# Kernel tuning notes

Measured on AMD Instinct MI355X. Metric: run time of the kernel, lower is better.

## Reference

```python
import jax, jax.numpy as jnp
import numpy as np

P = 16          # patch_size
EMBED = 768     # embed_dim
HEAD_DIM = 64   # embed_dim // num_heads
ROPE_BASE = 10000.0


def rope_2d(coords, head_dim, base):
    """Axial 2D RoPE. coords: (N, 2) int -> cos, sin each (N, head_dim).
    head_dim is split evenly over the two axes; within an axis, frequency
    pairs are repeated twice (standard rotate-pairs layout)."""
    dpa = head_dim // 2                                   # dims per axis
    inv_freq = 1.0 / (base ** (jnp.arange(0, dpa, 2, dtype=jnp.float32) / dpa))  # (dpa//2,)
    ang = coords.astype(jnp.float32)[:, :, None] * inv_freq[None, None, :]       # (N, 2, dpa//2)
    ang = jnp.repeat(ang, 2, axis=-1).reshape(coords.shape[0], head_dim)          # (N, head_dim)
    return jnp.cos(ang), jnp.sin(ang)


def setup_inputs() -> dict:
    key = jax.random.key(0)
    k1, k2 = jax.random.split(key, 2)
    B, C, H, W = 32, 3, 512, 512
    images = jax.random.normal(k1, (B, C, H, W), dtype=jnp.float32)
    patch_dim = C * P * P
    W_proj = jax.random.normal(k2, (patch_dim, EMBED), dtype=jnp.float32) * (patch_dim ** -0.5)
    b_proj = jnp.zeros((EMBED,), dtype=jnp.float32)
    return {"images": images, "W_proj": W_proj, "b_proj": b_proj}


def reference(images, W_proj, b_proj):
    B, C, H, W = images.shape
    Hp, Wp = H // P, W // P
    N = B * Hp * Wp
    # patchify: c (hp p1) (wp p2) -> (hp wp) (c p1 p2), packed across batch
    x = images.reshape(B, C, Hp, P, Wp, P).transpose(0, 2, 4, 1, 3, 5).reshape(N, C * P * P)
    tokens = x @ W_proj + b_proj                              # (N, EMBED)
    # per-image patch coordinates (identical grid for every image)
    ys, xs = jnp.meshgrid(jnp.arange(Hp), jnp.arange(Wp), indexing='ij')
    coords = jnp.stack([ys, xs], axis=-1).reshape(Hp * Wp, 2)
    patch_coords = jnp.tile(coords, (B, 1))                    # (N, 2)
    rope_cos, rope_sin = rope_2d(patch_coords, HEAD_DIM, ROPE_BASE)
    cu_seqlens = (jnp.arange(B + 1, dtype=jnp.int32) * (Hp * Wp))
    is_patch = jnp.ones((N,), dtype=bool)
    return tokens, cu_seqlens, patch_coords, rope_cos, rope_sin, is_patch
```

## Files before the change

kernel.cpp:

```cpp
#include <hip/hip_runtime.h>
#include <hip/hip_bf16.h>

typedef unsigned short u16;
typedef unsigned int   u32;
typedef __bf16 bf16x8 __attribute__((ext_vector_type(8)));
typedef float  f32x4  __attribute__((ext_vector_type(4)));

#define N_TOK 32768
constexpr long long OFF_TOKENS = 0;
constexpr long long OFF_CU     = 25165824LL;
constexpr long long OFF_COORDS = 25165857LL;
constexpr long long OFF_COS    = 25231393LL;
constexpr long long OFF_SIN    = 27328545LL;
constexpr long long OFF_ISP    = 29425697LL;

__device__ __forceinline__ void split_bf16(float v, u16& h, u16& l) {
    __hip_bfloat16 bh = __float2bfloat16(v);
    float fh = __bfloat162float(bh);
    __hip_bfloat16 bl = __float2bfloat16(v - fh);
    h = __builtin_bit_cast(u16, bh);
    l = __builtin_bit_cast(u16, bl);
}

__device__ __forceinline__ u32 pk2(float lo, float hi) {
    u32 a = (u32)__builtin_bit_cast(u16, __float2bfloat16(lo));
    u32 b = (u32)__builtin_bit_cast(u16, __float2bfloat16(hi));
    return a | (b << 16);
}

__global__ __launch_bounds__(256) void prep_w(const float* __restrict__ W,
                                              u16* __restrict__ wt2) {
    const int bid = blockIdx.x;
    const int bn  = bid / 24;
    const int kt  = bid - bn * 24;
    __shared__ u16 im[8192];
    const int t  = threadIdx.x;
    const int k  = t >> 3;
    const int n0 = (t & 7) * 16;
    const float* src = W + (size_t)(kt * 32 + k) * 768 + bn * 128 + n0;
    #pragma unroll
    for (int e = 0; e < 16; e++) {
        const int n = n0 + e;
        u16 h, l;
        split_bf16(src[e], h, l);
        const int p = (n * 64 + (((k >> 4) ^ ((n >> 3) & 1)) << 5) + (k & 15) * 2) >> 1;
        im[p] = h;
        im[4096 + p] = l;
    }
    __syncthreads();
    uint4* g = (uint4*)(wt2 + (size_t)bid * 8192);
    const uint4* s = (const uint4*)im;
    #pragma unroll
    for (int i = 0; i < 4; i++) g[t + i * 256] = s[t + i * 256];
}

__global__ __launch_bounds__(512, 4) void patch_gemm_mfma(
    const float* __restrict__ img, const u16* __restrict__ wt2,
    const float* __restrict__ bias, float* __restrict__ out)
{
    __shared__ __align__(16) char smem[49152];
    char* pA0 = smem;
    char* pA1 = smem + 8192;
    char* pB0 = smem + 16384;
    char* pB1 = smem + 32768;

    const int L   = blockIdx.x;
    const int c   = (L & 7) * 192 + (L >> 3);
    const int bm  = c / 6;
    const int bn  = c - bm * 6;
    const int tb  = bn * 24;

    const int tid  = threadIdx.x;
    const int lane = tid & 63;
    const int wid  = tid >> 6;
    const int wm   = (wid >> 2) << 6;
    const int wn   = (wid & 3) << 5;
    const int lr   = lane & 15;
    const int lg   = lane >> 4;

    const int am = tid & 127;
    const int aq = tid >> 7;
    const int m  = bm * 128 + am;
    const int bb = m >> 10;
    const int hp = (m & 1023) >> 5;
    const int wq = m & 31;
    const float* abase = img + (size_t)bb * 786432 + (size_t)hp * 8192 + wq * 16;
    const int a_wb = am * 64 + (((aq >> 1) ^ ((am >> 3) & 1)) << 5) + ((aq & 1) << 4);

    const int a_rd = lr * 64 + (((lg >> 1) ^ ((lr >> 3) & 1)) << 5) + ((lg & 1) << 4);

    f32x4 acc[4][2];
    #pragma unroll
    for (int i = 0; i < 4; i++)
        #pragma unroll
        for (int j = 0; j < 2; j++) acc[i][j] = {0.f, 0.f, 0.f, 0.f};

    float4 A0a, A0b, A1a, A1b;

#define LOAD_A(ra, rb, T)                                                   \
    {   const float* ap = abase + ((T) >> 3) * 262144 +                     \
            (((T) & 7) * 2 + (aq >> 1)) * 512 + (aq & 1) * 8;               \
        ra = *(const float4*)ap;  rb = *(const float4*)(ap + 4); }

#define CVT_STORE(ra, rb, pdst)                                             \
    {   uint4 Hq;                                                           \
        Hq.x = pk2(ra.x, ra.y); Hq.y = pk2(ra.z, ra.w);                     \
        Hq.z = pk2(rb.x, rb.y); Hq.w = pk2(rb.z, rb.w);                     \
        *(uint4*)((pdst) + a_wb) = Hq; }

#define GLOADB(T, dst)                                                      \
    {   const char* s = (const char*)wt2 + (size_t)(tb + (T)) * 16384       \
                        + (wid << 11) + (lane << 4);                        \
        char* d = (dst) + (wid << 11);                                      \
        __builtin_amdgcn_global_load_lds(                                   \
            (const __attribute__((address_space(1))) u32*)s,                \
            (__attribute__((address_space(3))) u32*)d, 16, 0, 0);           \
        __builtin_amdgcn_global_load_lds(                                   \
            (const __attribute__((address_space(1))) u32*)(s + 1024),       \
            (__attribute__((address_space(3))) u32*)(d + 1024), 16, 0, 0); }

#define COMPUTE(pAc, pBc)                                                   \
    {   bf16x8 ahf[4], bhf[2], blf[2];                                      \
        _Pragma("unroll")                                                   \
        for (int i = 0; i < 4; i++)                                         \
            ahf[i] = *(const bf16x8*)((pAc) + ((wm + i * 16) << 6) + a_rd); \
        _Pragma("unroll")                                                   \
        for (int j = 0; j < 2; j++) {                                       \
            bhf[j] = *(const bf16x8*)((pBc) + ((wn + j * 16) << 6) + a_rd); \
            blf[j] = *(const bf16x8*)((pBc) + 8192 + ((wn + j * 16) << 6) + a_rd); \
        }                                                                   \
        _Pragma("unroll")                                                   \
        for (int i = 0; i < 4; i++)                                         \
            _Pragma("unroll")                                               \
            for (int j = 0; j < 2; j++) {                                   \
                acc[i][j] = __builtin_amdgcn_mfma_f32_16x16x32_bf16(ahf[i], bhf[j], acc[i][j], 0, 0, 0); \
                acc[i][j] = __builtin_amdgcn_mfma_f32_16x16x32_bf16(ahf[i], blf[j], acc[i][j], 0, 0, 0); \
            } }

    LOAD_A(A0a, A0b, 0);
    GLOADB(0, pB0);
    LOAD_A(A1a, A1b, 1);
    CVT_STORE(A0a, A0b, pA0);
    __syncthreads();

    #pragma unroll 1
    for (int t = 0; t < 24; t += 2) {
        if (t < 23) { CVT_STORE(A1a, A1b, pA1); GLOADB(t + 1, pB1); }
        if (t < 22) LOAD_A(A0a, A0b, t + 2);
        COMPUTE(pA0, pB0);
        __syncthreads();
        if (t + 1 < 23) { CVT_STORE(A0a, A0b, pA0); GLOADB(t + 2, pB0); }
        if (t + 1 < 22) LOAD_A(A1a, A1b, t + 3);
        COMPUTE(pA1, pB1);
        __syncthreads();
    }
#undef LOAD_A
#undef CVT_STORE
#undef GLOADB
#undef COMPUTE

    float bv[2];
    #pragma unroll
    for (int j = 0; j < 2; j++) bv[j] = bias[bn * 128 + wn + j * 16 + lr];
    #pragma unroll
    for (int i = 0; i < 4; i++) {
        const int rb = bm * 128 + wm + i * 16 + lg * 4;
        #pragma unroll
        for (int j = 0; j < 2; j++) {
            const int cg = bn * 128 + wn + j * 16 + lr;
            #pragma unroll
            for (int r = 0; r < 4; r++)
                out[OFF_TOKENS + (size_t)(rb + r) * 768 + cg] = acc[i][j][r] + bv[j];
        }
    }
}

__global__ __launch_bounds__(256) void aux_kernel(float* __restrict__ out)
{
    const int idx = blockIdx.x * 256 + threadIdx.x;
    if (idx >= N_TOK * 32) return;
    const int n  = idx >> 5;
    const int jd = idx & 31;

    const int hp = (n & 1023) >> 5;
    const int wp = n & 31;

    const int coord = (jd < 16) ? hp : wp;
    const int j = jd & 15;
    const float freq = exp2f(-(float)j * 0.8304820237218406f);
    float s, c;
    sincosf((float)coord * freq, &s, &c);

    const long long off = (long long)n * 64 + jd * 2;
    *(float2*)(out + OFF_COS + off) = make_float2(c, c);
    *(float2*)(out + OFF_SIN + off) = make_float2(s, s);

    if (jd == 0) {
        out[OFF_COORDS + 2 * (long long)n]     = (float)hp;
        out[OFF_COORDS + 2 * (long long)n + 1] = (float)wp;
        out[OFF_ISP + n] = 1.0f;
    }
    if (jd == 1 && n < 33) {
        out[OFF_CU + n] = (float)(n * 1024);
    }
}

extern "C" void kernel_launch(void* const* d_in, const int* in_sizes, int n_in,
                              void* d_out, int out_size, void* d_ws, size_t ws_size,
                              hipStream_t stream) {
    const float* img  = (const float*)d_in[0];
    const float* W    = (const float*)d_in[1];
    const float* bias = (const float*)d_in[2];
    float* out = (float*)d_out;
    u16* wt2 = (u16*)d_ws;

    prep_w<<<144, 256, 0, stream>>>(W, wt2);

    patch_gemm_mfma<<<1536, 512, 0, stream>>>(img, wt2, bias, out);

    const int aux_elems = N_TOK * 32;
    aux_kernel<<<(aux_elems + 255) / 256, 256, 0, stream>>>(out);
}
```

Before: 266.8 us.

## Triple-buffer GEMM LDS tiles with deeper prefetch and explicit waitcnt barriers

```diff
diff --git a/kernel.cpp b/kernel.cpp
--- a/kernel.cpp
+++ b/kernel.cpp
@@ -58,11 +58,13 @@
     const float* __restrict__ img, const u16* __restrict__ wt2,
     const float* __restrict__ bias, float* __restrict__ out)
 {
-    __shared__ __align__(16) char smem[49152];
+    __shared__ __align__(16) char smem[73728];
     char* pA0 = smem;
     char* pA1 = smem + 8192;
-    char* pB0 = smem + 16384;
-    char* pB1 = smem + 32768;
+    char* pA2 = smem + 16384;
+    char* pB0 = smem + 24576;
+    char* pB1 = smem + 40960;
+    char* pB2 = smem + 57344;
 
     const int L   = blockIdx.x;
     const int c   = (L & 7) * 192 + (L >> 3);
@@ -95,7 +97,7 @@
         #pragma unroll
         for (int j = 0; j < 2; j++) acc[i][j] = {0.f, 0.f, 0.f, 0.f};
 
-    float4 A0a, A0b, A1a, A1b;
+    float4 A0a, A0b, A1a, A1b, A2a, A2b;
 
 #define LOAD_A(ra, rb, T)                                                   \
     {   const float* ap = abase + ((T) >> 3) * 262144 +                     \
@@ -137,23 +139,32 @@
                 acc[i][j] = __builtin_amdgcn_mfma_f32_16x16x32_bf16(ahf[i], blf[j], acc[i][j], 0, 0, 0); \
             } }
 
+#define ITER(T, Ca, Cb, La, Lb, PACV, PBGL, PAC, PBC)                       \
+    {   if ((T) + 1 < 24) CVT_STORE(Ca, Cb, PACV);                          \
+        if ((T) + 2 < 24) GLOADB((T) + 2, PBGL);                            \
+        __builtin_amdgcn_sched_barrier(0);                                  \
+        if ((T) + 3 < 24) LOAD_A(La, Lb, (T) + 3);                          \
+        COMPUTE(PAC, PBC);                                                  \
+        asm volatile("s_waitcnt vmcnt(6) lgkmcnt(0)" ::: "memory");         \
+        __builtin_amdgcn_s_barrier();                                       \
+    }
+
+    GLOADB(0, pB0);
     LOAD_A(A0a, A0b, 0);
-    GLOADB(0, pB0);
+    GLOADB(1, pB1);
     LOAD_A(A1a, A1b, 1);
+    LOAD_A(A2a, A2b, 2);
     CVT_STORE(A0a, A0b, pA0);
-    __syncthreads();
+    asm volatile("s_waitcnt vmcnt(6) lgkmcnt(0)" ::: "memory");
+    __builtin_amdgcn_s_barrier();
 
     #pragma unroll 1
-    for (int t = 0; t < 24; t += 2) {
-        if (t < 23) { CVT_STORE(A1a, A1b, pA1); GLOADB(t + 1, pB1); }
-        if (t < 22) LOAD_A(A0a, A0b, t + 2);
-        COMPUTE(pA0, pB0);
-        __syncthreads();
-        if (t + 1 < 23) { CVT_STORE(A0a, A0b, pA0); GLOADB(t + 2, pB0); }
-        if (t + 1 < 22) LOAD_A(A1a, A1b, t + 3);
-        COMPUTE(pA1, pB1);
-        __syncthreads();
-    }
+    for (int t = 0; t < 24; t += 3) {
+        ITER(t,     A1a, A1b, A0a, A0b, pA1, pB2, pA0, pB0);
+        ITER(t + 1, A2a, A2b, A1a, A1b, pA2, pB0, pA1, pB1);
+        ITER(t + 2, A0a, A0b, A2a, A2b, pA0, pB1, pA2, pB2);
+    }
+#undef ITER
 #undef LOAD_A
 #undef CVT_STORE
 #undef GLOADB
```

After: 263.1 us. About the same (-1.4%).

## Load W fragments directly from global into registers, dropping B LDS staging

Applied to the files above, without the earlier changes.

```diff
diff --git a/kernel.cpp b/kernel.cpp
--- a/kernel.cpp
+++ b/kernel.cpp
@@ -33,36 +33,37 @@
     const int bid = blockIdx.x;
     const int bn  = bid / 24;
     const int kt  = bid - bn * 24;
-    __shared__ u16 im[8192];
-    const int t  = threadIdx.x;
-    const int k  = t >> 3;
-    const int n0 = (t & 7) * 16;
-    const float* src = W + (size_t)(kt * 32 + k) * 768 + bn * 128 + n0;
-    #pragma unroll
-    for (int e = 0; e < 16; e++) {
-        const int n = n0 + e;
-        u16 h, l;
-        split_bf16(src[e], h, l);
-        const int p = (n * 64 + (((k >> 4) ^ ((n >> 3) & 1)) << 5) + (k & 15) * 2) >> 1;
-        im[p] = h;
-        im[4096 + p] = l;
-    }
-    __syncthreads();
-    uint4* g = (uint4*)(wt2 + (size_t)bid * 8192);
-    const uint4* s = (const uint4*)im;
-    #pragma unroll
-    for (int i = 0; i < 4; i++) g[t + i * 256] = s[t + i * 256];
+    const int t   = threadIdx.x;
+    #pragma unroll
+    for (int p = 0; p < 2; p++) {
+        const int idx  = t + p * 256;
+        const int lane = idx & 63;
+        const int j    = (idx >> 6) & 1;
+        const int wnq  = idx >> 7;
+        const int n    = bn * 128 + wnq * 32 + j * 16 + (lane & 15);
+        const int k0   = kt * 32 + (lane >> 4) * 8;
+        u16 hv[8], lv[8];
+        #pragma unroll
+        for (int e = 0; e < 8; e++)
+            split_bf16(W[(size_t)(k0 + e) * 768 + n], hv[e], lv[e]);
+        uint4 H, L;
+        H.x = (u32)hv[0] | ((u32)hv[1] << 16); H.y = (u32)hv[2] | ((u32)hv[3] << 16);
+        H.z = (u32)hv[4] | ((u32)hv[5] << 16); H.w = (u32)hv[6] | ((u32)hv[7] << 16);
+        L.x = (u32)lv[0] | ((u32)lv[1] << 16); L.y = (u32)lv[2] | ((u32)lv[3] << 16);
+        L.z = (u32)lv[4] | ((u32)lv[5] << 16); L.w = (u32)lv[6] | ((u32)lv[7] << 16);
+        u16* dst = wt2 + (size_t)bid * 8192 + (((wnq << 12) | (j << 10) | (lane << 4)) >> 1);
+        *(uint4*)dst          = H;
+        *(uint4*)(dst + 1024) = L;
+    }
 }
 
 __global__ __launch_bounds__(512, 4) void patch_gemm_mfma(
     const float* __restrict__ img, const u16* __restrict__ wt2,
     const float* __restrict__ bias, float* __restrict__ out)
 {
-    __shared__ __align__(16) char smem[49152];
+    __shared__ __align__(16) char smem[16384];
     char* pA0 = smem;
     char* pA1 = smem + 8192;
-    char* pB0 = smem + 16384;
-    char* pB1 = smem + 32768;
 
     const int L   = blockIdx.x;
     const int c   = (L & 7) * 192 + (L >> 3);
@@ -89,6 +90,8 @@
 
     const int a_rd = lr * 64 + (((lg >> 1) ^ ((lr >> 3) & 1)) << 5) + ((lg & 1) << 4);
 
+    const char* bfrag = (const char*)wt2 + ((wid & 3) << 12) + (lane << 4);
+
     f32x4 acc[4][2];
     #pragma unroll
     for (int i = 0; i < 4; i++)
@@ -108,56 +111,44 @@
         Hq.z = pk2(rb.x, rb.y); Hq.w = pk2(rb.z, rb.w);                     \
         *(uint4*)((pdst) + a_wb) = Hq; }
 
-#define GLOADB(T, dst)                                                      \
-    {   const char* s = (const char*)wt2 + (size_t)(tb + (T)) * 16384       \
-                        + (wid << 11) + (lane << 4);                        \
-        char* d = (dst) + (wid << 11);                                      \
-        __builtin_amdgcn_global_load_lds(                                   \
-            (const __attribute__((address_space(1))) u32*)s,                \
-            (__attribute__((address_space(3))) u32*)d, 16, 0, 0);           \
-        __builtin_amdgcn_global_load_lds(                                   \
-            (const __attribute__((address_space(1))) u32*)(s + 1024),       \
-            (__attribute__((address_space(3))) u32*)(d + 1024), 16, 0, 0); }
-
-#define COMPUTE(pAc, pBc)                                                   \
-    {   bf16x8 ahf[4], bhf[2], blf[2];                                      \
+#define ITER(T, Ca, Cb, La, Lb, PACV, PAC)                                  \
+    {   bf16x8 bhf[2], blf[2];                                              \
+        {   const char* s = bfrag + (size_t)(tb + (T)) * 16384;             \
+            bhf[0] = *(const bf16x8*)(s);                                   \
+            bhf[1] = *(const bf16x8*)(s + 1024);                            \
+            blf[0] = *(const bf16x8*)(s + 2048);                            \
+            blf[1] = *(const bf16x8*)(s + 3072); }                          \
+        if ((T) + 1 < 24) CVT_STORE(Ca, Cb, PACV);                          \
+        if ((T) + 2 < 24) LOAD_A(La, Lb, (T) + 2);                          \
+        bf16x8 ahf[4];                                                      \
         _Pragma("unroll")                                                   \
         for (int i = 0; i < 4; i++)                                         \
-            ahf[i] = *(const bf16x8*)((pAc) + ((wm + i * 16) << 6) + a_rd); \
-        _Pragma("unroll")                                                   \
-        for (int j = 0; j < 2; j++) {                                       \
-            bhf[j] = *(const bf16x8*)((pBc) + ((wn + j * 16) << 6) + a_rd); \
-            blf[j] = *(const bf16x8*)((pBc) + 8192 + ((wn + j * 16) << 6) + a_rd); \
-        }                                                                   \
+            ahf[i] = *(const bf16x8*)((PAC) + ((wm + i * 16) << 6) + a_rd); \
         _Pragma("unroll")                                                   \
         for (int i = 0; i < 4; i++)                                         \
             _Pragma("unroll")                                               \
             for (int j = 0; j < 2; j++) {                                   \
                 acc[i][j] = __builtin_amdgcn_mfma_f32_16x16x32_bf16(ahf[i], bhf[j], acc[i][j], 0, 0, 0); \
                 acc[i][j] = __builtin_amdgcn_mfma_f32_16x16x32_bf16(ahf[i], blf[j], acc[i][j], 0, 0, 0); \
-            } }
+            }                                                               \
+        asm volatile("s_waitcnt lgkmcnt(0)" ::: "memory");                  \
+        __builtin_amdgcn_s_barrier();                                       \
+    }
 
     LOAD_A(A0a, A0b, 0);
-    GLOADB(0, pB0);
     LOAD_A(A1a, A1b, 1);
     CVT_STORE(A0a, A0b, pA0);
-    __syncthreads();
+    asm volatile("s_waitcnt lgkmcnt(0)" ::: "memory");
+    __builtin_amdgcn_s_barrier();
 
     #pragma unroll 1
     for (int t = 0; t < 24; t += 2) {
-        if (t < 23) { CVT_STORE(A1a, A1b, pA1); GLOADB(t + 1, pB1); }
-        if (t < 22) LOAD_A(A0a, A0b, t + 2);
-        COMPUTE(pA0, pB0);
-        __syncthreads();
-        if (t + 1 < 23) { CVT_STORE(A0a, A0b, pA0); GLOADB(t + 2, pB0); }
-        if (t + 1 < 22) LOAD_A(A1a, A1b, t + 3);
-        COMPUTE(pA1, pB1);
-        __syncthreads();
-    }
+        ITER(t,     A1a, A1b, A0a, A0b, pA1, pA0);
+        ITER(t + 1, A0a, A0b, A1a, A1b, pA0, pA1);
+    }
+#undef ITER
 #undef LOAD_A
 #undef CVT_STORE
-#undef GLOADB
-#undef COMPUTE
 
     float bv[2];
     #pragma unroll
```

Measured after the change: 275.7 us. 1.03x slower.
